# Performance work log

Hardware: AMD Instinct MI355X
Metric: run time of the kernel (lower is better)

Reference implementation:

```python
import jax, jax.numpy as jnp
import numpy as np

C = 256; G = 16; GC = C // G; K = 3; P = K * K
N = 4; H = 64; W = 64
PAD = 1; OFFSET_SCALE = 1.0; LN_EPS = 1e-5


def setup_inputs() -> dict:
    key = jax.random.key(0)
    ks = jax.random.split(key, 8)
    s = 0.02
    return {
        "x": jax.random.normal(ks[0], (N, C, H, W), jnp.float32),
        "dw_w": jax.random.normal(ks[1], (C, 1, K, K), jnp.float32) * s,
        "dw_b": jnp.zeros((C,), jnp.float32),
        "ln_g": jnp.ones((C,), jnp.float32),
        "ln_b": jnp.zeros((C,), jnp.float32),
        "off_w": jax.random.normal(ks[2], (C, G * P * 2), jnp.float32) * s,
        "off_b": jnp.zeros((G * P * 2,), jnp.float32),
        "mask_w": jax.random.normal(ks[3], (C, G * P), jnp.float32) * s,
        "mask_b": jnp.zeros((G * P,), jnp.float32),
        "inp_w": jax.random.normal(ks[4], (C, C), jnp.float32) * s,
        "inp_b": jnp.zeros((C,), jnp.float32),
        "out_w": jax.random.normal(ks[5], (C, C), jnp.float32) * s,
        "out_b": jnp.zeros((C,), jnp.float32),
    }


def _dcnv3_nchw(x, dw_w, dw_b, ln_g, ln_b, off_w, off_b, mask_w, mask_b,
                inp_w, inp_b, out_w, out_b):
    # NCHW -> NHWC (wrapper permute)
    xn = jnp.transpose(x, (0, 2, 3, 1))                      # (N,H,W,C)
    x_proj = xn @ inp_w + inp_b                              # input_proj

    # offset/mask branch: depthwise conv (NCHW) -> LayerNorm (channels-last) -> GELU
    x1 = jax.lax.conv_general_dilated(
        x, dw_w, window_strides=(1, 1), padding=((PAD, PAD), (PAD, PAD)),
        dimension_numbers=("NCHW", "OIHW", "NCHW"), feature_group_count=C)
    x1 = jnp.transpose(x1, (0, 2, 3, 1)) + dw_b
    mu = x1.mean(-1, keepdims=True)
    var = ((x1 - mu) ** 2).mean(-1, keepdims=True)
    x1 = (x1 - mu) * jax.lax.rsqrt(var + LN_EPS) * ln_g + ln_b
    x1 = jax.nn.gelu(x1, approximate=False)

    offset = (x1 @ off_w + off_b).reshape(N, H, W, G, P, 2)  # (x,y) pairs
    mask = jax.nn.softmax((x1 @ mask_w + mask_b).reshape(N, H, W, G, P), axis=-1)

    # pad sampled feature map with zeros (F.pad before sampling)
    xp = jnp.pad(x_proj, ((0, 0), (PAD, PAD), (PAD, PAD), (0, 0)))
    Hin, Win = H + 2 * PAD, W + 2 * PAD
    xg = xp.reshape(N, Hin, Win, G, GC)

    # reference points, normalized by padded size
    ref_y = (jnp.arange(H, dtype=jnp.float32) + PAD + 0.5) / Hin
    ref_x = (jnp.arange(W, dtype=jnp.float32) + PAD + 0.5) / Win
    ref = jnp.stack([jnp.broadcast_to(ref_x[None, :], (H, W)),
                     jnp.broadcast_to(ref_y[:, None], (H, W))], -1)  # (H,W,2)

    # dilation grid: x varies in the outer loop (torch meshgrid 'ij')
    d = jnp.arange(K, dtype=jnp.float32) - (K - 1) // 2     # [-1,0,1]
    gx = jnp.repeat(d, K) / Win
    gy = jnp.tile(d, K) / Hin
    grid = jnp.stack([gx, gy], -1)                           # (P,2)

    norm = jnp.array([Win, Hin], jnp.float32)
    loc = (ref[None, :, :, None, None, :] + grid * OFFSET_SCALE
           + offset * OFFSET_SCALE / norm)                   # (N,H,W,G,P,2)

    # grid_sample bilinear, align_corners=False, zero padding
    px = loc[..., 0] * Win - 0.5
    py = loc[..., 1] * Hin - 0.5
    x0 = jnp.floor(px); y0 = jnp.floor(py)
    wx = px - x0; wy = py - y0
    x0i = x0.astype(jnp.int32); y0i = y0.astype(jnp.int32)

    n_idx = jnp.arange(N)[:, None, None, None, None]
    g_idx = jnp.arange(G)[None, None, None, :, None]

    def corner(iy, ix, w):
        valid = (iy >= 0) & (iy < Hin) & (ix >= 0) & (ix < Win)
        v = xg[n_idx, jnp.clip(iy, 0, Hin - 1), jnp.clip(ix, 0, Win - 1), g_idx]
        wgt = jnp.where(valid, w, 0.0) * mask                # fold mask into weights
        return jnp.einsum("nhwgp,nhwgpc->nhwgc", wgt, v)

    out = (corner(y0i, x0i, (1 - wy) * (1 - wx))
           + corner(y0i, x0i + 1, (1 - wy) * wx)
           + corner(y0i + 1, x0i, wy * (1 - wx))
           + corner(y0i + 1, x0i + 1, wy * wx))               # (N,H,W,G,GC)

    out = out.reshape(N, H, W, C) @ out_w + out_b            # output_proj
    return jnp.transpose(out, (0, 3, 1, 2))                  # NHWC -> NCHW


def reference(x, dw_w, dw_b, ln_g, ln_b, off_w, off_b, mask_w, mask_b,
              inp_w, inp_b, out_w, out_b):
    return _dcnv3_nchw(x, dw_w, dw_b, ln_g, ln_b, off_w, off_b,
                       mask_w, mask_b, inp_w, inp_b, out_w, out_b)
```

## Files before the change

kernel.cpp:

```cpp
#include <hip/hip_runtime.h>
#include <hip/hip_bf16.h>
#include <math.h>


using bf16x8 = __attribute__((ext_vector_type(8))) short;
using f32x4  = __attribute__((ext_vector_type(4))) float;

#define GLOBAL_AS __attribute__((address_space(1)))
#define LDS_AS    __attribute__((address_space(3)))

static __device__ inline void g2lds16(const void* g, void* l) {
  __builtin_amdgcn_global_load_lds((const GLOBAL_AS int*)g, (LDS_AS int*)l, 16, 0, 0);
}
static __device__ inline unsigned short f2bf(float v) {
  __hip_bfloat16 b = __float2bfloat16(v);
  return *reinterpret_cast<unsigned short*>(&b);
}
static __device__ inline float us2f(unsigned short u) {
  union { unsigned u; float f; } c; c.u = ((unsigned)u) << 16; return c.f;
}

__global__ __launch_bounds__(256) void prep_w_k(
    const float* __restrict__ inp_w, const float* __restrict__ off_w,
    const float* __restrict__ off_b, const float* __restrict__ mask_w,
    const float* __restrict__ mask_b, const float* __restrict__ out_w,
    __hip_bfloat16* __restrict__ BtI, __hip_bfloat16* __restrict__ BtOM,
    __hip_bfloat16* __restrict__ BtO, float* __restrict__ bOM)
{
  const int b = blockIdx.x, t = threadIdx.x;
  if (b < 256) {
    int n = b;
    BtI[n * 256 + t] = __float2bfloat16(inp_w[t * 256 + n]);
  } else if (b < 768) {
    int n = b - 256;
    float v = 0.f;
    if (n < 288) v = off_w[t * 288 + n];
    else if (n < 432) v = mask_w[t * 144 + (n - 288)];
    BtOM[n * 256 + t] = __float2bfloat16(v);
    if (b == 256) {
      for (int idx = t; idx < 512; idx += 256) {
        float bv = (idx < 288) ? off_b[idx] : ((idx < 432) ? mask_b[idx - 288] : 0.f);
        bOM[idx] = bv;
      }
    }
  } else {
    int n = b - 768;
    BtO[n * 256 + t] = __float2bfloat16(out_w[t * 256 + n]);
  }
}

__global__ __launch_bounds__(1024) void stage2_gi_k(
    const float* __restrict__ x,
    const float* __restrict__ dw_w, const float* __restrict__ dw_b,
    const float* __restrict__ ln_g, const float* __restrict__ ln_b,
    const __hip_bfloat16* __restrict__ BtI, const float* __restrict__ inp_b,
    __hip_bfloat16* __restrict__ xpu, __hip_bfloat16* __restrict__ x1g)
{
  __shared__ __align__(16) char smem[42496];
  const int bid = blockIdx.x;
  const int t = threadIdx.x;

  if (bid >= 256) {
    unsigned short* A = (unsigned short*)smem;
    float* ftile = (float*)(smem + 33792);

    const int strip = bid - 256;
    const int n4 = strip >> 6, hw0 = (strip & 63) * 64;
    const float* xb = x + (size_t)n4 * 1048576 + hw0;

    const int cl0 = t >> 6, wl0 = t & 63;
    const int cl1 = (t + 1024) >> 6, wl1 = (t + 1024) & 63;
    float p0 = xb[(size_t)cl0 * 4096 + wl0];
    float p1 = xb[(size_t)cl1 * 4096 + wl1];

    for (int ck = 0; ck < 8; ++ck) {
      const int ch0 = ck * 32;
      ftile[cl0 * 65 + wl0] = p0;
      ftile[cl1 * 65 + wl1] = p1;
      if (ck < 7) {
        p0 = xb[(size_t)(ch0 + 32 + cl0) * 4096 + wl0];
        p1 = xb[(size_t)(ch0 + 32 + cl1) * 4096 + wl1];
      }
      __syncthreads();
      {
        int px = t >> 4, cq2 = t & 15;
        unsigned short b0 = f2bf(ftile[(cq2 * 2) * 65 + px]);
        unsigned short b1 = f2bf(ftile[(cq2 * 2 + 1) * 65 + px]);
        *(unsigned*)&A[px * 264 + ch0 + cq2 * 2] =
            (unsigned)b0 | ((unsigned)b1 << 16);
      }
      __syncthreads();
    }

    const int wave = t >> 6, lane = t & 63;
    const int quad = lane >> 4, lr = lane & 15;
    const int wm = wave >> 2, wn = wave & 3;

    bf16x8 areg[8];
    #pragma unroll
    for (int s = 0; s < 8; ++s)
      areg[s] = *(const bf16x8*)&A[(wm * 16 + lr) * 264 + s * 32 + quad * 8];
    __syncthreads();

    auto stageI = [&](int s, int buf) {
      int col = t >> 2, kq = t & 3;
      g2lds16(BtI + (size_t)col * 256 + s * 32 + kq * 8,
              smem + buf * 16384 + t * 16);
    };

    f32x4 acc[4];
    #pragma unroll
    for (int i = 0; i < 4; ++i) acc[i] = (f32x4){0.f, 0.f, 0.f, 0.f};

    stageI(0, 0);
    __syncthreads();
    #pragma unroll
    for (int s = 0; s < 8; ++s) {
      if (s < 7) stageI(s + 1, (s + 1) & 1);
      const short* B = (const short*)(smem + (s & 1) * 16384);
      bf16x8 bfr[4];
      #pragma unroll
      for (int ni = 0; ni < 4; ++ni)
        bfr[ni] = *(const bf16x8*)&B[(wn * 64 + ni * 16 + lr) * 32 + quad * 8];
      #pragma unroll
      for (int ni = 0; ni < 4; ++ni)
        acc[ni] = __builtin_amdgcn_mfma_f32_16x16x32_bf16(areg[s], bfr[ni], acc[ni], 0, 0, 0);
      __syncthreads();
    }

    const size_t m0 = (size_t)strip * 64;
    #pragma unroll
    for (int ni = 0; ni < 4; ++ni) {
      int col = wn * 64 + ni * 16 + lr;
      float bv = inp_b[col];
      #pragma unroll
      for (int reg = 0; reg < 4; ++reg) {
        size_t m = m0 + wm * 16 + quad * 4 + reg;
        xpu[m * 256 + col] = __float2bfloat16(acc[ni][reg] + bv);
      }
    }
    return;
  }

  unsigned short* x1t = (unsigned short*)smem;
  float* psq  = (float*)(smem + 33792);
  float* murs = (float*)(smem + 41984);

  const int blk = ((bid & 7) << 5) | (bid >> 3);
  const int n4 = blk >> 6, h = blk & 63;
  const int w = t & 63, q = t >> 6;

  const float* xb = x + (size_t)n4 * 1048576;
  const bool hm = (h > 0), hp = (h < 63);
  float av[16];
  float s1 = 0.f, s2 = 0.f;

  #pragma unroll 2
  for (int j = 0; j < 8; ++j) {
    #pragma unroll
    for (int u = 0; u < 2; ++u) {
      const int c = q * 16 + 2 * j + u;
      const float* xc = xb + (size_t)c * 4096 + h * 64 + w;
      float v0 = hm ? xc[-64] : 0.f;
      float v1 = xc[0];
      float v2 = hp ? xc[64] : 0.f;
      const float* wp = dw_w + c * 9;
      float a = dw_b[c];
      #pragma unroll
      for (int dh = 0; dh < 3; ++dh) {
        float v = (dh == 0) ? v0 : (dh == 1) ? v1 : v2;
        float vm = __shfl(v, w - 1, 64);
        float vp = __shfl(v, w + 1, 64);
        if (w == 0)  vm = 0.f;
        if (w == 63) vp = 0.f;
        a = fmaf(vm, wp[dh * 3 + 0], a);
        a = fmaf(v,  wp[dh * 3 + 1], a);
        a = fmaf(vp, wp[dh * 3 + 2], a);
      }
      s1 += a;
      s2 = fmaf(a, a, s2);
      av[2 * j + u] = a;
    }
  }

  psq[q * 64 + w] = s1;
  psq[1024 + q * 64 + w] = s2;
  __syncthreads();
  if (t < 64) {
    float a = 0.f, b = 0.f;
    #pragma unroll
    for (int j = 0; j < 16; ++j) { a += psq[j * 64 + t]; b += psq[1024 + j * 64 + t]; }
    float mu = a * (1.f / 256.f);
    murs[t] = mu;
    murs[64 + t] = rsqrtf(b * (1.f / 256.f) - mu * mu + 1e-5f);
  }
  __syncthreads();
  {
    float mu = murs[w], rs = murs[64 + w];
    #pragma unroll
    for (int j = 0; j < 8; ++j) {
      int c = q * 16 + 2 * j;
      float y0 = fmaf((av[2 * j] - mu) * rs, ln_g[c], ln_b[c]);
      float y1 = fmaf((av[2 * j + 1] - mu) * rs, ln_g[c + 1], ln_b[c + 1]);
      float g0 = 0.5f * y0 * (1.f + erff(y0 * 0.70710678f));
      float g1 = 0.5f * y1 * (1.f + erff(y1 * 0.70710678f));
      *(unsigned*)&x1t[w * 264 + c] = (unsigned)f2bf(g0) | ((unsigned)f2bf(g1) << 16);
    }
  }
  __syncthreads();

  const size_t pix0 = (size_t)n4 * 4096 + (size_t)h * 64;
  #pragma unroll
  for (int r = 0; r < 2; ++r) {
    int j = t + r * 1024;
    int px = j >> 5, cu = j & 31;
    *(uint4*)&x1g[(pix0 + px) * 256 + cu * 8] = *(const uint4*)&x1t[px * 264 + cu * 8];
  }
}

__global__ __launch_bounds__(512) void fused_so_k(
    const __hip_bfloat16* __restrict__ x1g, const __hip_bfloat16* __restrict__ xpu,
    const __hip_bfloat16* __restrict__ BtOM, const float* __restrict__ bOM,
    const __hip_bfloat16* __restrict__ BtO, const float* __restrict__ out_b,
    float* __restrict__ out)
{
  __shared__ __align__(16) char smem[78336];
  unsigned short* x1s = (unsigned short*)smem;
  unsigned short* st  = (unsigned short*)smem;
  unsigned short* Som = (unsigned short*)(smem + 16896);

  const int bid = blockIdx.x;
  const int swz = ((bid & 7) << 6) | (bid >> 3);
  const int pix0 = swz << 5;
  const int t = threadIdx.x;

  const int wave = t >> 6, lane = t & 63;
  const int quad = lane >> 4, lr = lane & 15;
  const int wm = wave >> 2, wn = wave & 3;

  auto stageB = [&](int s, int buf) {
    char* dst = smem + 16896 + buf * 28672;
    #pragma unroll
    for (int r = 0; r < 3; ++r) {
      int j = t + r * 512;
      int col = j >> 2, kq = j & 3;
      g2lds16(BtOM + (size_t)col * 256 + s * 32 + kq * 8, dst + j * 16);
    }
    if (t < 256) {
      int j = t + 1536;
      int col = j >> 2, kq = j & 3;
      g2lds16(BtOM + (size_t)col * 256 + s * 32 + kq * 8, dst + j * 16);
    }
  };
  auto stageO = [&](int s, int buf) {
    char* dst = smem + 45568 + buf * 16384;
    #pragma unroll
    for (int r = 0; r < 2; ++r) {
      int j = t + r * 512;
      int col = j >> 2, kq = j & 3;
      g2lds16(BtO + (size_t)col * 256 + s * 32 + kq * 8, dst + j * 16);
    }
  };

  #pragma unroll
  for (int r = 0; r < 2; ++r) {
    int j = t + r * 512;
    int px = j >> 5, cu = j & 31;
    g2lds16(x1g + (size_t)(pix0 + px) * 256 + cu * 8, smem + j * 16);
  }
  stageB(0, 0);
  __syncthreads();

  bf16x8 areg[8];
  #pragma unroll
  for (int s = 0; s < 8; ++s)
    areg[s] = *(const bf16x8*)&x1s[(wm * 16 + lr) * 256 + s * 32 + quad * 8];

  f32x4 acc[7];
  #pragma unroll
  for (int i = 0; i < 7; ++i) acc[i] = (f32x4){0.f, 0.f, 0.f, 0.f};

  #pragma unroll
  for (int s = 0; s < 8; ++s) {
    if (s < 7) stageB(s + 1, (s + 1) & 1);
    const short* B = (const short*)(smem + 16896 + (s & 1) * 28672);
    bf16x8 bfr[7];
    #pragma unroll
    for (int ni = 0; ni < 7; ++ni)
      bfr[ni] = *(const bf16x8*)&B[(wn * 112 + ni * 16 + lr) * 32 + quad * 8];
    #pragma unroll
    for (int ni = 0; ni < 7; ++ni)
      acc[ni] = __builtin_amdgcn_mfma_f32_16x16x32_bf16(areg[s], bfr[ni], acc[ni], 0, 0, 0);
    __syncthreads();
  }

  #pragma unroll
  for (int ni = 0; ni < 7; ++ni) {
    int col = wn * 112 + ni * 16 + lr;
    float bv = bOM[col];
    #pragma unroll
    for (int reg = 0; reg < 4; ++reg) {
      int m = wm * 16 + quad * 4 + reg;
      Som[m * 448 + col] = f2bf(acc[ni][reg] + bv);
    }
  }
  __syncthreads();

  stageO(0, 0);

  {
    const int pl = t >> 4, g = t & 15;
    const int pix = pix0 + pl;
    const int n4s = pix >> 12;
    const int hw = pix & 4095;
    const int h = hw >> 6, w = hw & 63;
    const unsigned short* omp = Som + pl * 448;

    float mk[9];
    {
      float mx = -1e30f;
      #pragma unroll
      for (int p = 0; p < 9; ++p) { mk[p] = us2f(omp[288 + g * 9 + p]); mx = fmaxf(mx, mk[p]); }
      float se = 0.f;
      #pragma unroll
      for (int p = 0; p < 9; ++p) { mk[p] = __expf(mk[p] - mx); se += mk[p]; }
      float inv = 1.f / se;
      #pragma unroll
      for (int p = 0; p < 9; ++p) mk[p] *= inv;
    }

    const __hip_bfloat16* xpg = xpu + (g << 4);
    float ax[16];
    #pragma unroll
    for (int i = 0; i < 16; ++i) ax[i] = 0.f;

    auto corner = [&](int iy, int ix, float wt) {
      if ((unsigned)(iy - 1) >= 64u || (unsigned)(ix - 1) >= 64u) return;
      const __hip_bfloat16* src =
          xpg + ((size_t)((n4s << 12) + (iy - 1) * 64 + (ix - 1)) << 8);
      uint4 u0 = *(const uint4*)src;
      uint4 u1 = *(const uint4*)(src + 8);
      const unsigned uu[8] = {u0.x, u0.y, u0.z, u0.w, u1.x, u1.y, u1.z, u1.w};
      #pragma unroll
      for (int i = 0; i < 8; ++i) {
        float lo = us2f((unsigned short)(uu[i] & 0xffff));
        float hi = us2f((unsigned short)(uu[i] >> 16));
        ax[2 * i + 0] = fmaf(wt, lo, ax[2 * i + 0]);
        ax[2 * i + 1] = fmaf(wt, hi, ax[2 * i + 1]);
      }
    };

    #pragma unroll
    for (int p = 0; p < 9; ++p) {
      float ox = us2f(omp[g * 18 + 2 * p]), oy = us2f(omp[g * 18 + 2 * p + 1]);
      float px = (float)(w + p / 3) + ox;
      float py = (float)(h + p % 3) + oy;
      float xf = floorf(px), yf = floorf(py);
      float wx = px - xf, wy = py - yf;
      int ix = (int)xf, iy = (int)yf;
      float m = mk[p];
      corner(iy,     ix,     (1.f - wy) * (1.f - wx) * m);
      corner(iy,     ix + 1, (1.f - wy) * wx * m);
      corner(iy + 1, ix,     wy * (1.f - wx) * m);
      corner(iy + 1, ix + 1, wy * wx * m);
    }

    unsigned short ub[16];
    #pragma unroll
    for (int i = 0; i < 16; ++i) ub[i] = f2bf(ax[i]);
    uint4 u0, u1;
    u0.x = (unsigned)ub[0] | ((unsigned)ub[1] << 16);
    u0.y = (unsigned)ub[2] | ((unsigned)ub[3] << 16);
    u0.z = (unsigned)ub[4] | ((unsigned)ub[5] << 16);
    u0.w = (unsigned)ub[6] | ((unsigned)ub[7] << 16);
    u1.x = (unsigned)ub[8] | ((unsigned)ub[9] << 16);
    u1.y = (unsigned)ub[10] | ((unsigned)ub[11] << 16);
    u1.z = (unsigned)ub[12] | ((unsigned)ub[13] << 16);
    u1.w = (unsigned)ub[14] | ((unsigned)ub[15] << 16);
    *(uint4*)&st[pl * 264 + g * 16] = u0;
    *(uint4*)&st[pl * 264 + g * 16 + 8] = u1;
  }
  __syncthreads();

  bf16x8 areg2[8];
  #pragma unroll
  for (int s = 0; s < 8; ++s)
    areg2[s] = *(const bf16x8*)&st[(wm * 16 + lr) * 264 + s * 32 + quad * 8];

  f32x4 acc2[4];
  #pragma unroll
  for (int i = 0; i < 4; ++i) acc2[i] = (f32x4){0.f, 0.f, 0.f, 0.f};

  #pragma unroll
  for (int s = 0; s < 8; ++s) {
    if (s < 7) stageO(s + 1, (s + 1) & 1);
    const short* B = (const short*)(smem + 45568 + (s & 1) * 16384);
    bf16x8 bfr[4];
    #pragma unroll
    for (int ni = 0; ni < 4; ++ni)
      bfr[ni] = *(const bf16x8*)&B[(wn * 64 + ni * 16 + lr) * 32 + quad * 8];
    #pragma unroll
    for (int ni = 0; ni < 4; ++ni)
      acc2[ni] = __builtin_amdgcn_mfma_f32_16x16x32_bf16(areg2[s], bfr[ni], acc2[ni], 0, 0, 0);
    __syncthreads();
  }

  const int n4 = pix0 >> 12, hw0 = pix0 & 4095;
  #pragma unroll
  for (int ni = 0; ni < 4; ++ni) {
    int col = wn * 64 + ni * 16 + lr;
    float bv = out_b[col];
    float4 v;
    v.x = acc2[ni][0] + bv; v.y = acc2[ni][1] + bv;
    v.z = acc2[ni][2] + bv; v.w = acc2[ni][3] + bv;
    *(float4*)&out[(size_t)(n4 * 256 + col) * 4096 + hw0 + wm * 16 + quad * 4] = v;
  }
}

extern "C" void kernel_launch(void* const* d_in, const int* in_sizes, int n_in,
                              void* d_out, int out_size, void* d_ws, size_t ws_size,
                              hipStream_t stream) {
  const float* x      = (const float*)d_in[0];
  const float* dw_w   = (const float*)d_in[1];
  const float* dw_b   = (const float*)d_in[2];
  const float* ln_g   = (const float*)d_in[3];
  const float* ln_b   = (const float*)d_in[4];
  const float* off_w  = (const float*)d_in[5];
  const float* off_b  = (const float*)d_in[6];
  const float* mask_w = (const float*)d_in[7];
  const float* mask_b = (const float*)d_in[8];
  const float* inp_w  = (const float*)d_in[9];
  const float* inp_b  = (const float*)d_in[10];
  const float* out_w  = (const float*)d_in[11];
  const float* out_b  = (const float*)d_in[12];
  float* out = (float*)d_out;

  char* w0 = (char*)d_ws;
  __hip_bfloat16* xpu  = (__hip_bfloat16*)(w0);
  __hip_bfloat16* x1g  = (__hip_bfloat16*)(w0 + 8388608);
  __hip_bfloat16* BtI  = (__hip_bfloat16*)(w0 + 16777216);
  __hip_bfloat16* BtOM = (__hip_bfloat16*)(w0 + 16908288);
  __hip_bfloat16* BtO  = (__hip_bfloat16*)(w0 + 17170432);
  float*          bOM  = (float*)(w0 + 17301504);
  if (ws_size < 17303552) return;

  prep_w_k<<<1024, 256, 0, stream>>>(inp_w, off_w, off_b, mask_w, mask_b,
                                     out_w, BtI, BtOM, BtO, bOM);
  stage2_gi_k<<<512, 1024, 0, stream>>>(x, dw_w, dw_b, ln_g, ln_b,
                                        BtI, inp_b, xpu, x1g);
  fused_so_k<<<512, 512, 0, stream>>>(x1g, xpu, BtOM, bOM, BtO, out_b, out);
}
```

Baseline: 147.0 us.

## Fuse input projection GEMM into depthwise-conv kernel, reusing loaded x values

Each block now handles 32 pixels and runs both the depthwise conv + LayerNorm + GELU branch and the input-projection GEMM. Previously these were done by separate block groups, and the GEMM blocks reread and transposed x through shared memory. The center-tap values already loaded for the conv are packed to bf16 and used directly as the GEMM A tile, so x is read from global memory once instead of twice. In exchange, the conv needs extra boundary loads at the half-row edges, and blocks are smaller with fewer threads and more sequential work per block.

New measurement: 148.8 us. Within noise of the previous version (+1.3%).

```diff
diff --git a/kernel.cpp b/kernel.cpp
--- a/kernel.cpp
+++ b/kernel.cpp
@@ -49,106 +49,27 @@
   }
 }
 
-__global__ __launch_bounds__(1024) void stage2_gi_k(
+__global__ __launch_bounds__(512) void conv_gi_k(
     const float* __restrict__ x,
     const float* __restrict__ dw_w, const float* __restrict__ dw_b,
     const float* __restrict__ ln_g, const float* __restrict__ ln_b,
     const __hip_bfloat16* __restrict__ BtI, const float* __restrict__ inp_b,
     __hip_bfloat16* __restrict__ xpu, __hip_bfloat16* __restrict__ x1g)
 {
-  __shared__ __align__(16) char smem[42496];
+  __shared__ __align__(16) char smem[38144];
+  unsigned short* A   = (unsigned short*)smem;
+  unsigned short* x1t = (unsigned short*)(smem + 16896);
+  float* psq  = (float*)(smem + 33792);
+  float* murs = (float*)(smem + 37888);
+
   const int bid = blockIdx.x;
+  const int blk = ((bid & 7) << 6) | (bid >> 3);
+  const int pix0 = blk << 5;
+  const int n4 = pix0 >> 12, hw = pix0 & 4095;
+  const int h = hw >> 6, w0 = hw & 63;
   const int t = threadIdx.x;
-
-  if (bid >= 256) {
-    unsigned short* A = (unsigned short*)smem;
-    float* ftile = (float*)(smem + 33792);
-
-    const int strip = bid - 256;
-    const int n4 = strip >> 6, hw0 = (strip & 63) * 64;
-    const float* xb = x + (size_t)n4 * 1048576 + hw0;
-
-    const int cl0 = t >> 6, wl0 = t & 63;
-    const int cl1 = (t + 1024) >> 6, wl1 = (t + 1024) & 63;
-    float p0 = xb[(size_t)cl0 * 4096 + wl0];
-    float p1 = xb[(size_t)cl1 * 4096 + wl1];
-
-    for (int ck = 0; ck < 8; ++ck) {
-      const int ch0 = ck * 32;
-      ftile[cl0 * 65 + wl0] = p0;
-      ftile[cl1 * 65 + wl1] = p1;
-      if (ck < 7) {
-        p0 = xb[(size_t)(ch0 + 32 + cl0) * 4096 + wl0];
-        p1 = xb[(size_t)(ch0 + 32 + cl1) * 4096 + wl1];
-      }
-      __syncthreads();
-      {
-        int px = t >> 4, cq2 = t & 15;
-        unsigned short b0 = f2bf(ftile[(cq2 * 2) * 65 + px]);
-        unsigned short b1 = f2bf(ftile[(cq2 * 2 + 1) * 65 + px]);
-        *(unsigned*)&A[px * 264 + ch0 + cq2 * 2] =
-            (unsigned)b0 | ((unsigned)b1 << 16);
-      }
-      __syncthreads();
-    }
-
-    const int wave = t >> 6, lane = t & 63;
-    const int quad = lane >> 4, lr = lane & 15;
-    const int wm = wave >> 2, wn = wave & 3;
-
-    bf16x8 areg[8];
-    #pragma unroll
-    for (int s = 0; s < 8; ++s)
-      areg[s] = *(const bf16x8*)&A[(wm * 16 + lr) * 264 + s * 32 + quad * 8];
-    __syncthreads();
-
-    auto stageI = [&](int s, int buf) {
-      int col = t >> 2, kq = t & 3;
-      g2lds16(BtI + (size_t)col * 256 + s * 32 + kq * 8,
-              smem + buf * 16384 + t * 16);
-    };
-
-    f32x4 acc[4];
-    #pragma unroll
-    for (int i = 0; i < 4; ++i) acc[i] = (f32x4){0.f, 0.f, 0.f, 0.f};
-
-    stageI(0, 0);
-    __syncthreads();
-    #pragma unroll
-    for (int s = 0; s < 8; ++s) {
-      if (s < 7) stageI(s + 1, (s + 1) & 1);
-      const short* B = (const short*)(smem + (s & 1) * 16384);
-      bf16x8 bfr[4];
-      #pragma unroll
-      for (int ni = 0; ni < 4; ++ni)
-        bfr[ni] = *(const bf16x8*)&B[(wn * 64 + ni * 16 + lr) * 32 + quad * 8];
-      #pragma unroll
-      for (int ni = 0; ni < 4; ++ni)
-        acc[ni] = __builtin_amdgcn_mfma_f32_16x16x32_bf16(areg[s], bfr[ni], acc[ni], 0, 0, 0);
-      __syncthreads();
-    }
-
-    const size_t m0 = (size_t)strip * 64;
-    #pragma unroll
-    for (int ni = 0; ni < 4; ++ni) {
-      int col = wn * 64 + ni * 16 + lr;
-      float bv = inp_b[col];
-      #pragma unroll
-      for (int reg = 0; reg < 4; ++reg) {
-        size_t m = m0 + wm * 16 + quad * 4 + reg;
-        xpu[m * 256 + col] = __float2bfloat16(acc[ni][reg] + bv);
-      }
-    }
-    return;
-  }
-
-  unsigned short* x1t = (unsigned short*)smem;
-  float* psq  = (float*)(smem + 33792);
-  float* murs = (float*)(smem + 41984);
-
-  const int blk = ((bid & 7) << 5) | (bid >> 3);
-  const int n4 = blk >> 6, h = blk & 63;
-  const int w = t & 63, q = t >> 6;
+  const int px = t & 31, q = t >> 5;
+  const int lane = t & 63;
 
   const float* xb = x + (size_t)n4 * 1048576;
   const bool hm = (h > 0), hp = (h < 63);
@@ -157,10 +78,11 @@
 
   #pragma unroll 2
   for (int j = 0; j < 8; ++j) {
+    unsigned pk = 0;
     #pragma unroll
     for (int u = 0; u < 2; ++u) {
       const int c = q * 16 + 2 * j + u;
-      const float* xc = xb + (size_t)c * 4096 + h * 64 + w;
+      const float* xc = xb + (size_t)c * 4096 + h * 64 + w0 + px;
       float v0 = hm ? xc[-64] : 0.f;
       float v1 = xc[0];
       float v2 = hp ? xc[64] : 0.f;
@@ -168,35 +90,38 @@
       float a = dw_b[c];
       #pragma unroll
       for (int dh = 0; dh < 3; ++dh) {
-        float v = (dh == 0) ? v0 : (dh == 1) ? v1 : v2;
-        float vm = __shfl(v, w - 1, 64);
-        float vp = __shfl(v, w + 1, 64);
-        if (w == 0)  vm = 0.f;
-        if (w == 63) vp = 0.f;
+        const bool rok = (dh == 1) || (dh == 0 ? hm : hp);
+        float vv = (dh == 0) ? v0 : (dh == 1) ? v1 : v2;
+        float vm = __shfl(vv, lane - 1, 64);
+        float vp = __shfl(vv, lane + 1, 64);
+        if (px == 0)  vm = (rok && w0 > 0)  ? xc[(dh - 1) * 64 - 1] : 0.f;
+        if (px == 31) vp = (rok && w0 < 32) ? xc[(dh - 1) * 64 + 1] : 0.f;
         a = fmaf(vm, wp[dh * 3 + 0], a);
-        a = fmaf(v,  wp[dh * 3 + 1], a);
+        a = fmaf(vv, wp[dh * 3 + 1], a);
         a = fmaf(vp, wp[dh * 3 + 2], a);
       }
       s1 += a;
       s2 = fmaf(a, a, s2);
       av[2 * j + u] = a;
-    }
-  }
-
-  psq[q * 64 + w] = s1;
-  psq[1024 + q * 64 + w] = s2;
-  __syncthreads();
-  if (t < 64) {
+      pk |= ((unsigned)f2bf(v1)) << (16 * u);
+    }
+    *(unsigned*)&A[px * 264 + q * 16 + 2 * j] = pk;
+  }
+
+  psq[t] = s1;
+  psq[512 + t] = s2;
+  __syncthreads();
+  if (t < 32) {
     float a = 0.f, b = 0.f;
     #pragma unroll
-    for (int j = 0; j < 16; ++j) { a += psq[j * 64 + t]; b += psq[1024 + j * 64 + t]; }
+    for (int j = 0; j < 16; ++j) { a += psq[j * 32 + t]; b += psq[512 + j * 32 + t]; }
     float mu = a * (1.f / 256.f);
     murs[t] = mu;
-    murs[64 + t] = rsqrtf(b * (1.f / 256.f) - mu * mu + 1e-5f);
+    murs[32 + t] = rsqrtf(b * (1.f / 256.f) - mu * mu + 1e-5f);
   }
   __syncthreads();
   {
-    float mu = murs[w], rs = murs[64 + w];
+    float mu = murs[px], rs = murs[32 + px];
     #pragma unroll
     for (int j = 0; j < 8; ++j) {
       int c = q * 16 + 2 * j;
@@ -204,17 +129,65 @@
       float y1 = fmaf((av[2 * j + 1] - mu) * rs, ln_g[c + 1], ln_b[c + 1]);
       float g0 = 0.5f * y0 * (1.f + erff(y0 * 0.70710678f));
       float g1 = 0.5f * y1 * (1.f + erff(y1 * 0.70710678f));
-      *(unsigned*)&x1t[w * 264 + c] = (unsigned)f2bf(g0) | ((unsigned)f2bf(g1) << 16);
-    }
-  }
-  __syncthreads();
-
-  const size_t pix0 = (size_t)n4 * 4096 + (size_t)h * 64;
+      *(unsigned*)&x1t[px * 264 + c] = (unsigned)f2bf(g0) | ((unsigned)f2bf(g1) << 16);
+    }
+  }
+  __syncthreads();
+
   #pragma unroll
   for (int r = 0; r < 2; ++r) {
-    int j = t + r * 1024;
-    int px = j >> 5, cu = j & 31;
-    *(uint4*)&x1g[(pix0 + px) * 256 + cu * 8] = *(const uint4*)&x1t[px * 264 + cu * 8];
+    int jj = t + r * 512;
+    int pxl = jj >> 5, cu = jj & 31;
+    *(uint4*)&x1g[(size_t)(pix0 + pxl) * 256 + cu * 8] =
+        *(const uint4*)&x1t[pxl * 264 + cu * 8];
+  }
+  const int quad = lane >> 4, lr = lane & 15;
+  const int wave = t >> 6, wm = wave >> 2, wn = wave & 3;
+  bf16x8 areg[8];
+  #pragma unroll
+  for (int s = 0; s < 8; ++s)
+    areg[s] = *(const bf16x8*)&A[(wm * 16 + lr) * 264 + s * 32 + quad * 8];
+  __syncthreads();
+
+  auto stageI = [&](int s, int buf) {
+    char* dst = smem + buf * 16384;
+    #pragma unroll
+    for (int r = 0; r < 2; ++r) {
+      int j = t + r * 512;
+      int col = j >> 2, kq = j & 3;
+      g2lds16(BtI + (size_t)col * 256 + s * 32 + kq * 8, dst + j * 16);
+    }
+  };
+
+  f32x4 acc[4];
+  #pragma unroll
+  for (int i = 0; i < 4; ++i) acc[i] = (f32x4){0.f, 0.f, 0.f, 0.f};
+
+  stageI(0, 0);
+  __syncthreads();
+  #pragma unroll
+  for (int s = 0; s < 8; ++s) {
+    if (s < 7) stageI(s + 1, (s + 1) & 1);
+    const short* B = (const short*)(smem + (s & 1) * 16384);
+    bf16x8 bfr[4];
+    #pragma unroll
+    for (int ni = 0; ni < 4; ++ni)
+      bfr[ni] = *(const bf16x8*)&B[(wn * 64 + ni * 16 + lr) * 32 + quad * 8];
+    #pragma unroll
+    for (int ni = 0; ni < 4; ++ni)
+      acc[ni] = __builtin_amdgcn_mfma_f32_16x16x32_bf16(areg[s], bfr[ni], acc[ni], 0, 0, 0);
+    __syncthreads();
+  }
+
+  #pragma unroll
+  for (int ni = 0; ni < 4; ++ni) {
+    int col = wn * 64 + ni * 16 + lr;
+    float bv = inp_b[col];
+    #pragma unroll
+    for (int reg = 0; reg < 4; ++reg) {
+      size_t m = (size_t)pix0 + wm * 16 + quad * 4 + reg;
+      xpu[m * 256 + col] = __float2bfloat16(acc[ni][reg] + bv);
+    }
   }
 }
 
@@ -446,7 +419,7 @@
 
   prep_w_k<<<1024, 256, 0, stream>>>(inp_w, off_w, off_b, mask_w, mask_b,
                                      out_w, BtI, BtOM, BtO, bOM);
-  stage2_gi_k<<<512, 1024, 0, stream>>>(x, dw_w, dw_b, ln_g, ln_b,
-                                        BtI, inp_b, xpu, x1g);
+  conv_gi_k<<<512, 512, 0, stream>>>(x, dw_w, dw_b, ln_g, ln_b,
+                                     BtI, inp_b, xpu, x1g);
   fused_so_k<<<512, 512, 0, stream>>>(x1g, xpu, BtOM, bOM, BtO, out_b, out);
 }
```
